# Optimization experiments

Measured on AMD Instinct MI355X. Metric: run time of the kernel, lower is better.

## Reference

```python
import jax, jax.numpy as jnp
import numpy as np

CLAMP_MAX = 20.0
N, T, I = 32, 128, 128


def setup_inputs() -> dict:
    key = jax.random.key(0)
    k_in, k_tg, k_nan = jax.random.split(key, 3)
    inp = jax.random.normal(k_in, (N, T, I), dtype=jnp.float32)
    tgt = (jax.random.uniform(k_tg, (N, T, I)) > 0.5).astype(jnp.float32)
    nan_mask = jax.random.uniform(k_nan, (N, T, I)) < 0.2
    tgt = jnp.where(nan_mask, jnp.nan, tgt)
    return {"input": inp, "target": tgt}


def reference(input, target):
    is_not_nan = ~jnp.isnan(target)                      # [N,T,I]
    new_target = jnp.where(is_not_nan, target * 2.0 - 1.0, 0.0)
    positive = new_target > 0                            # [N,T,I]
    negative = new_target < 0                            # [N,T,I]
    # item_pairs[n,t,i,j] = negative[i] & positive[j]
    item_pairs = (negative[..., :, None] & positive[..., None, :]).astype(input.dtype)
    # diff[n,t,i,j] = input[i] - input[j]
    diff = input[..., :, None] - input[..., None, :]     # [N,T,I,I]
    sp = jnp.log1p(jnp.exp(jnp.minimum(diff, CLAMP_MAX)))
    bpr = jnp.einsum('ntij,ntij->nt', sp, item_pairs)    # [N,T]
    row_valid = jnp.any(is_not_nan, axis=-1)             # [N,T]
    # mean over rows with at least one non-NaN label
    return jnp.sum(bpr * row_valid) / jnp.sum(row_valid.astype(bpr.dtype))
```

## Files before the change

### kernel.cpp

```cpp
#include <hip/hip_runtime.h>
#include <hip/hip_bf16.h>
#include <math.h>

#define NB 32
#define TB 128
#define IB 128
#define ROWS (NB * TB)
constexpr float CLAMP_MAX = 20.0f;
constexpr float LOG2E = 1.4426950408889634f;
constexpr float LN2   = 0.6931471805599453f;

__global__ __launch_bounds__(256) void bpr_row_kernel(
        const float* __restrict__ input,
        const float* __restrict__ target,
        float* __restrict__ sums,
        float* __restrict__ valid) {
    const int row = blockIdx.x;
    const float* in = input  + (size_t)row * IB;
    const float* tg = target + (size_t)row * IB;

    __shared__ float negV[IB];
    __shared__ float posV[IB];
    __shared__ int   cnts[2];
    __shared__ float wredu[4];

    const int tid  = threadIdx.x;
    const int wave = tid >> 6;
    const int lane = tid & 63;

    if (tid < 2) cnts[tid] = 0;
    __syncthreads();

    if (tid < IB) {
        float t = tg[tid];
        if (t == t) {
            float x = in[tid];
            if (t > 0.5f) { int p = atomicAdd(&cnts[1], 1); posV[p] = x; }
            else          { int p = atomicAdd(&cnts[0], 1); negV[p] = x; }
        }
    }
    __syncthreads();

    const int negC = cnts[0];
    const int posC = cnts[1];

    float acc = 0.0f;
    for (int i = wave; i < negC; i += 4) {
        const float nv = negV[i];
        for (int j = lane; j < posC; j += 64) {
            float d = fminf(nv - posV[j], CLAMP_MAX);
            float e = __builtin_amdgcn_exp2f(d * LOG2E);
            acc += __builtin_amdgcn_logf(1.0f + e) * LN2;
        }
    }

    #pragma unroll
    for (int off = 32; off > 0; off >>= 1)
        acc += __shfl_down(acc, off, 64);
    if (lane == 0) wredu[wave] = acc;
    __syncthreads();
    if (tid == 0) {
        const bool v = (negC + posC) > 0;
        sums[row]  = v ? (wredu[0] + wredu[1] + wredu[2] + wredu[3]) : 0.0f;
        valid[row] = v ? 1.0f : 0.0f;
    }
}

__global__ __launch_bounds__(256) void bpr_reduce_kernel(
        const float* __restrict__ sums,
        const float* __restrict__ valid,
        float* __restrict__ out) {
    const int tid  = threadIdx.x;
    const int wave = tid >> 6;
    const int lane = tid & 63;
    float s = 0.0f, c = 0.0f;
    for (int i = tid; i < ROWS; i += 256) {
        s += sums[i];
        c += valid[i];
    }
    #pragma unroll
    for (int off = 32; off > 0; off >>= 1) {
        s += __shfl_down(s, off, 64);
        c += __shfl_down(c, off, 64);
    }
    __shared__ float ss[4], cc[4];
    if (lane == 0) { ss[wave] = s; cc[wave] = c; }
    __syncthreads();
    if (tid == 0) {
        float S = ss[0] + ss[1] + ss[2] + ss[3];
        float C = cc[0] + cc[1] + cc[2] + cc[3];
        out[0] = S / C;
    }
}

extern "C" void kernel_launch(void* const* d_in, const int* in_sizes, int n_in,
                              void* d_out, int out_size, void* d_ws, size_t ws_size,
                              hipStream_t stream) {
    const float* input  = (const float*)d_in[0];
    const float* target = (const float*)d_in[1];
    float* out   = (float*)d_out;
    float* sums  = (float*)d_ws;
    float* valid = sums + ROWS;

    hipLaunchKernelGGL(bpr_row_kernel, dim3(ROWS), dim3(256), 0, stream,
                       input, target, sums, valid);
    hipLaunchKernelGGL(bpr_reduce_kernel, dim3(1), dim3(256), 0, stream,
                       sums, valid, out);
}
```

Measured before the change: 68.75 us.

## Map one wavefront per row with ballot-based compaction and unrolled pair loop

```diff
diff --git a/kernel.cpp b/kernel.cpp
--- a/kernel.cpp
+++ b/kernel.cpp
@@ -6,62 +6,74 @@
 #define TB 128
 #define IB 128
 #define ROWS (NB * TB)
+#define WPB 4
 constexpr float CLAMP_MAX = 20.0f;
 constexpr float LOG2E = 1.4426950408889634f;
 constexpr float LN2   = 0.6931471805599453f;
+
+__device__ __forceinline__ float softplus_clamped(float d) {
+    d = fminf(d, CLAMP_MAX);
+    float e = __builtin_amdgcn_exp2f(d * LOG2E);
+    return __builtin_amdgcn_logf(1.0f + e) * LN2;
+}
 
 __global__ __launch_bounds__(256) void bpr_row_kernel(
         const float* __restrict__ input,
         const float* __restrict__ target,
         float* __restrict__ sums,
         float* __restrict__ valid) {
-    const int row = blockIdx.x;
-    const float* in = input  + (size_t)row * IB;
-    const float* tg = target + (size_t)row * IB;
-
-    __shared__ float negV[IB];
-    __shared__ float posV[IB];
-    __shared__ int   cnts[2];
-    __shared__ float wredu[4];
+    __shared__ float negQ[WPB][IB];
+    __shared__ float posQ[WPB][IB];
 
     const int tid  = threadIdx.x;
     const int wave = tid >> 6;
     const int lane = tid & 63;
+    const int row  = blockIdx.x * WPB + wave;
 
-    if (tid < 2) cnts[tid] = 0;
-    __syncthreads();
+    const float2 x2 = ((const float2*)(input  + (size_t)row * IB))[lane];
+    const float2 t2 = ((const float2*)(target + (size_t)row * IB))[lane];
 
-    if (tid < IB) {
-        float t = tg[tid];
-        if (t == t) {
-            float x = in[tid];
-            if (t > 0.5f) { int p = atomicAdd(&cnts[1], 1); posV[p] = x; }
-            else          { int p = atomicAdd(&cnts[0], 1); negV[p] = x; }
+    const bool p0 = t2.x > 0.5f, p1 = t2.y > 0.5f;
+    const bool n0 = t2.x < 0.5f, n1 = t2.y < 0.5f;
+
+    const unsigned long long pm0 = __ballot(p0), pm1 = __ballot(p1);
+    const unsigned long long nm0 = __ballot(n0), nm1 = __ballot(n1);
+    const unsigned long long lt  = (1ULL << lane) - 1ULL;
+
+    const int posC = __popcll(pm0) + __popcll(pm1);
+    const int negC = __popcll(nm0) + __popcll(nm1);
+
+    float* nq = negQ[wave];
+    float* pq = posQ[wave];
+    if (n0) nq[__popcll(nm0 & lt)] = x2.x;
+    if (n1) nq[__popcll(nm0) + __popcll(nm1 & lt)] = x2.y;
+    if (p0) pq[__popcll(pm0 & lt)] = x2.x;
+    if (p1) pq[__popcll(pm0) + __popcll(pm1 & lt)] = x2.y;
+
+    float acc = 0.0f;
+    int i = 0;
+    for (; i + 4 <= negC; i += 4) {
+        const float a0 = nq[i], a1 = nq[i+1], a2 = nq[i+2], a3 = nq[i+3];
+        for (int j = lane; j < posC; j += 64) {
+            const float pv = pq[j];
+            acc += softplus_clamped(a0 - pv);
+            acc += softplus_clamped(a1 - pv);
+            acc += softplus_clamped(a2 - pv);
+            acc += softplus_clamped(a3 - pv);
         }
     }
-    __syncthreads();
-
-    const int negC = cnts[0];
-    const int posC = cnts[1];
-
-    float acc = 0.0f;
-    for (int i = wave; i < negC; i += 4) {
-        const float nv = negV[i];
-        for (int j = lane; j < posC; j += 64) {
-            float d = fminf(nv - posV[j], CLAMP_MAX);
-            float e = __builtin_amdgcn_exp2f(d * LOG2E);
-            acc += __builtin_amdgcn_logf(1.0f + e) * LN2;
-        }
+    for (; i < negC; ++i) {
+        const float a0 = nq[i];
+        for (int j = lane; j < posC; j += 64)
+            acc += softplus_clamped(a0 - pq[j]);
     }
 
     #pragma unroll
     for (int off = 32; off > 0; off >>= 1)
         acc += __shfl_down(acc, off, 64);
-    if (lane == 0) wredu[wave] = acc;
-    __syncthreads();
-    if (tid == 0) {
+    if (lane == 0) {
         const bool v = (negC + posC) > 0;
-        sums[row]  = v ? (wredu[0] + wredu[1] + wredu[2] + wredu[3]) : 0.0f;
+        sums[row]  = v ? acc : 0.0f;
         valid[row] = v ? 1.0f : 0.0f;
     }
 }
@@ -102,7 +114,7 @@
     float* sums  = (float*)d_ws;
     float* valid = sums + ROWS;
 
-    hipLaunchKernelGGL(bpr_row_kernel, dim3(ROWS), dim3(256), 0, stream,
+    hipLaunchKernelGGL(bpr_row_kernel, dim3(ROWS / WPB), dim3(256), 0, stream,
                        input, target, sums, valid);
     hipLaunchKernelGGL(bpr_reduce_kernel, dim3(1), dim3(256), 0, stream,
                        sums, valid, out);
```

Measured after the change: 66.16 us. 3.8% less time.
